# Performance work log

Measured on AMD Instinct MI355X. Metric: run time of the kernel, lower is better.

The kernel has to match this reference:

```python
import jax, jax.numpy as jnp
import numpy as np

# Dimensions (source globals scaled to production: r=256 residues, s=128 sequences)
S, R, CM, CZ, C, H = 128, 256, 256, 128, 32, 8
EPS = 1e-5  # torch LayerNorm default


def setup_inputs() -> dict:
    key = jax.random.key(0)
    ks = jax.random.split(key, 14)
    msa = jax.random.normal(ks[0], (S, R, CM), dtype=jnp.float32)
    pair = jax.random.normal(ks[1], (R, R, CZ), dtype=jnp.float32)
    u = lambda k, shape, fan: jax.random.uniform(k, shape, jnp.float32, -1.0 / np.sqrt(fan), 1.0 / np.sqrt(fan))
    return {
        "msa": msa,
        "pair": pair,
        # per-head LayerNorm affine params (stacked over head axis)
        "ln_msa_g": 1.0 + 0.1 * jax.random.normal(ks[2], (H, CM), dtype=jnp.float32),
        "ln_msa_b": 0.1 * jax.random.normal(ks[3], (H, CM), dtype=jnp.float32),
        "ln_pair_g": 1.0 + 0.1 * jax.random.normal(ks[4], (H, CZ), dtype=jnp.float32),
        "ln_pair_b": 0.1 * jax.random.normal(ks[5], (H, CZ), dtype=jnp.float32),
        # per-head projections (torch Linear without bias; stored as (in, out))
        "Wq": u(ks[6], (H, CM, C), CM),
        "Wk": u(ks[7], (H, CM, C), CM),
        "Wv": u(ks[8], (H, CM, C), CM),
        "Wg": u(ks[9], (H, CM, C), CM),
        "Wb": u(ks[10], (H, CZ, S), CZ),  # linear_b: c_z -> s
        # output projection c*H -> c_m (with bias)
        "Wo": u(ks[11], (H * C, CM), H * C),
        "bo": u(ks[12], (CM,), H * C),
    }


def _forward(msa, pair, ln_msa_g, ln_msa_b, ln_pair_g, ln_pair_b, Wq, Wk, Wv, Wg, Wb, Wo, bo):
    # LayerNorm normalization is head-independent; only affine differs per head.
    mu = msa.mean(-1, keepdims=True)
    var = msa.var(-1, keepdims=True)
    nm = (msa - mu) * jax.lax.rsqrt(var + EPS)              # (S, R, CM)
    p = nm[None] * ln_msa_g[:, None, None, :] + ln_msa_b[:, None, None, :]  # (H, S, R, CM)

    q = jnp.einsum("hsrc,hcd->hsrd", p, Wq)                  # (H, S, R, C)
    k = jnp.einsum("hsrc,hcd->hsrd", p, Wk)
    v = jnp.einsum("hsrc,hcd->hsrd", p, Wv)
    g = jax.nn.sigmoid(jnp.einsum("hsrc,hcd->hsrd", p, Wg))

    pmu = pair.mean(-1, keepdims=True)
    pvar = pair.var(-1, keepdims=True)
    npair = (pair - pmu) * jax.lax.rsqrt(pvar + EPS)         # (R, R, CZ)
    pp = npair[None] * ln_pair_g[:, None, None, :] + ln_pair_b[:, None, None, :]  # (H, R, R, CZ)
    bflat = jnp.einsum("hijc,hcs->hijs", pp, Wb)             # (H, R, R, S)
    # Faithful to torch: b = linear_b(flat_pair).view(s, r, r) -- a raw
    # row-major reinterpretation (NOT a transpose).
    b = bflat.reshape(H, S, R, R)

    inv_sqrt_c = np.float32(1.0 / np.sqrt(C))
    scores = (jnp.einsum("hsid,hsjd->hsij", q, k) + b) * inv_sqrt_c  # (H, S, R, R)
    # Source softmax is over dim=-2 (the query/row axis), faithful here.
    a = jax.nn.softmax(scores, axis=-2)
    o = g * jnp.einsum("hsij,hsjd->hsid", a, v)              # (H, S, R, C)

    # concat heads on last dim: (S, R, H*C)
    cat = jnp.transpose(o, (1, 2, 0, 3)).reshape(S, R, H * C)
    return cat @ Wo + bo                                      # (S, R, CM)


def reference(msa, pair, ln_msa_g, ln_msa_b, ln_pair_g, ln_pair_b, Wq, Wk, Wv, Wg, Wb, Wo, bo):
    return _forward(msa, pair, ln_msa_g, ln_msa_b, ln_pair_g, ln_pair_b, Wq, Wk, Wv, Wg, Wb, Wo, bo)
```

## Files before the change

kernel.cpp:

```cpp
#include <hip/hip_runtime.h>
#include <hip/hip_bf16.h>


namespace {
constexpr int S_ = 128, R_ = 256, CM_ = 256, CZ_ = 128, C_ = 32, H_ = 8;
constexpr int SR_ = S_ * R_;
constexpr int RR_ = R_ * R_;
constexpr float EPS_ = 1e-5f;
constexpr float ISC_ = 0.17677669529663687f;

constexpr size_t OFF_MU_M = 0;
constexpr size_t OFF_RS_M = OFF_MU_M + SR_;
constexpr size_t OFF_MU_P = OFF_RS_M + SR_;
constexpr size_t OFF_RS_P = OFF_MU_P + RR_;
constexpr size_t OFF_WC   = OFF_RS_P + RR_;
constexpr size_t OFF_BC   = OFF_WC + (size_t)H_ * CM_ * 128;
constexpr size_t OFF_WBP  = OFF_BC + (size_t)H_ * 128;
constexpr size_t OFF_BBP  = OFF_WBP + (size_t)H_ * CZ_ * 128;
constexpr size_t F32_END  = OFF_BBP + (size_t)H_ * 128;
constexpr size_t BF_BASE  = F32_END * 4;
constexpr size_t QKVG_ELEMS = (size_t)H_ * SR_ * C_;
constexpr size_t CAT_ELEMS  = (size_t)SR_ * CM_;
constexpr size_t WBT_ELEMS  = (size_t)H_ * 128 * 128;
constexpr size_t WOT_ELEMS  = (size_t)256 * 256;
constexpr size_t NEED_BYTES =
    BF_BASE + (4 * QKVG_ELEMS + CAT_ELEMS + WBT_ELEMS + WOT_ELEMS) * 2;
}

typedef unsigned short bf_t;
typedef short s8v __attribute__((ext_vector_type(8)));
typedef float f4v __attribute__((ext_vector_type(4)));

__device__ __forceinline__ unsigned pk2(float lo, float hi) {
  __hip_bfloat162 t = __float22bfloat162_rn(float2{lo, hi});
  return *reinterpret_cast<unsigned*>(&t);
}
__device__ __forceinline__ bf_t pk1(float v) {
  __hip_bfloat16 t = __float2bfloat16(v);
  return *reinterpret_cast<bf_t*>(&t);
}
__device__ __forceinline__ float uplo(unsigned u) { return __uint_as_float(u << 16); }
__device__ __forceinline__ float uphi(unsigned u) { return __uint_as_float(u & 0xffff0000u); }
__device__ __forceinline__ void up8(uint4 u, float* f) {
  f[0] = uplo(u.x); f[1] = uphi(u.x);
  f[2] = uplo(u.y); f[3] = uphi(u.y);
  f[4] = uplo(u.z); f[5] = uphi(u.z);
  f[6] = uplo(u.w); f[7] = uphi(u.w);
}
__device__ __forceinline__ f4v mfma16(s8v a, s8v b, f4v c) {
  return __builtin_amdgcn_mfma_f32_16x16x32_bf16(a, b, c, 0, 0, 0);
}

__global__ void msa_stats_k(const float* __restrict__ msa, float* __restrict__ mu,
                            float* __restrict__ rstd) {
  int row = blockIdx.x * 4 + (threadIdx.x >> 6);
  int lane = threadIdx.x & 63;
  float4 v = reinterpret_cast<const float4*>(msa + (size_t)row * CM_)[lane];
  float s = v.x + v.y + v.z + v.w;
  float s2 = v.x * v.x + v.y * v.y + v.z * v.z + v.w * v.w;
  for (int off = 32; off; off >>= 1) {
    s += __shfl_down(s, off);
    s2 += __shfl_down(s2, off);
  }
  if (lane == 0) {
    float m = s / CM_;
    float var = s2 / CM_ - m * m;
    mu[row] = m;
    rstd[row] = rsqrtf(var + EPS_);
  }
}

__global__ void pair_stats_k(const float* __restrict__ pair, float* __restrict__ mu,
                             float* __restrict__ rstd) {
  int row = blockIdx.x * 4 + (threadIdx.x >> 6);
  int lane = threadIdx.x & 63;
  float2 v = reinterpret_cast<const float2*>(pair + (size_t)row * CZ_)[lane];
  float s = v.x + v.y;
  float s2 = v.x * v.x + v.y * v.y;
  for (int off = 32; off; off >>= 1) {
    s += __shfl_down(s, off);
    s2 += __shfl_down(s2, off);
  }
  if (lane == 0) {
    float m = s / CZ_;
    float var = s2 / CZ_ - m * m;
    mu[row] = m;
    rstd[row] = rsqrtf(var + EPS_);
  }
}

__global__ void prep_weights_k(const float* __restrict__ lng_m, const float* __restrict__ lnb_m,
                               const float* __restrict__ lng_p, const float* __restrict__ lnb_p,
                               const float* __restrict__ Wq, const float* __restrict__ Wk,
                               const float* __restrict__ Wv, const float* __restrict__ Wg,
                               const float* __restrict__ Wb, const float* __restrict__ Wo,
                               bf_t* __restrict__ wct, float* __restrict__ bc,
                               float* __restrict__ Wbp, float* __restrict__ bbp,
                               bf_t* __restrict__ wbt, bf_t* __restrict__ wot) {
  int b = blockIdx.x;
  int t = threadIdx.x;
  if (b < H_) {
    int h = b;
    int m = t >> 5, d = t & 31;
    const float* Wsrc = (m == 0) ? Wq : (m == 1) ? Wk : (m == 2) ? Wv : Wg;
    float scale = (m == 0) ? ISC_ : 1.0f;
    float bias = 0.f;
    for (int c = 0; c < CM_; c++) {
      float w = Wsrc[((size_t)h * CM_ + c) * C_ + d];
      bias += lnb_m[h * CM_ + c] * w;
      wct[((size_t)h * 128 + t) * 256 + c] = pk1(lng_m[h * CM_ + c] * w * scale);
    }
    bc[h * 128 + t] = bias * scale;
  } else if (b < 2 * H_) {
    int h = b - H_;
    float bias = 0.f;
    for (int c = 0; c < CZ_; c++) {
      float w = Wb[((size_t)h * CZ_ + c) * S_ + t];
      bias += lnb_p[h * CZ_ + c] * w;
      Wbp[((size_t)h * CZ_ + c) * 128 + t] = lng_p[h * CZ_ + c] * w * ISC_;
    }
    bbp[h * 128 + t] = bias * ISC_;
    for (int c = 0; c < CZ_; c++)
      wbt[((size_t)h * 128 + t) * 128 + c] = pk1(Wbp[((size_t)h * CZ_ + c) * 128 + t]);
  } else {
    int n = (b - 2 * H_) * 128 + t;
    for (int k = 0; k < 256; k++) wot[(size_t)n * 256 + k] = pk1(Wo[(size_t)k * 256 + n]);
  }
}

__global__ __launch_bounds__(512, 1) void qkvg_mfma_k(
    const float* __restrict__ msa, const float* __restrict__ mu, const float* __restrict__ rstd,
    const bf_t* __restrict__ wct, const float* __restrict__ bc, bf_t* __restrict__ q,
    bf_t* __restrict__ k, bf_t* __restrict__ v, bf_t* __restrict__ g) {
  __shared__ bf_t sm_a[128 * 256];
  __shared__ bf_t sm_w[128 * 256];
  int ib = blockIdx.x;
  int tid = threadIdx.x;
  int w = tid >> 6, l = tid & 63;
  int l15 = l & 15, l4 = l >> 4;
  int iw = w >> 2, jw = w & 3;
  int sr0 = ib * 128;
  int sx7 = l15 & 7;
#pragma unroll
  for (int rep = 0; rep < 8; rep++) {
    int flat = rep * 512 + tid;
    int row = flat >> 5, c = flat & 31;
    int srow = sr0 + row;
    const float4* ps = reinterpret_cast<const float4*>(msa + (size_t)srow * CM_ + c * 8);
    float4 x0 = ps[0], x1 = ps[1];
    float m = mu[srow], rs = rstd[srow];
    uint4 wv;
    wv.x = pk2((x0.x - m) * rs, (x0.y - m) * rs);
    wv.y = pk2((x0.z - m) * rs, (x0.w - m) * rs);
    wv.z = pk2((x1.x - m) * rs, (x1.y - m) * rs);
    wv.w = pk2((x1.z - m) * rs, (x1.w - m) * rs);
    *reinterpret_cast<uint4*>(&sm_a[row * 256 + ((c ^ (row & 7)) << 3)]) = wv;
  }
  for (int h = 0; h < H_; h++) {
    __syncthreads();
#pragma unroll
    for (int rep = 0; rep < 8; rep++) {
      int flat = rep * 512 + tid;
      int row = flat >> 5, c = flat & 31;
      *reinterpret_cast<uint4*>(&sm_w[row * 256 + ((c ^ (row & 7)) << 3)]) =
          *reinterpret_cast<const uint4*>(wct + ((size_t)h * 128 + row) * 256 + c * 8);
    }
    f4v acc[4][2];
#pragma unroll
    for (int jt = 0; jt < 2; jt++) {
      float bb = bc[h * 128 + jw * 32 + jt * 16 + l15];
#pragma unroll
      for (int it = 0; it < 4; it++) acc[it][jt] = f4v{bb, bb, bb, bb};
    }
    __syncthreads();
#pragma unroll
    for (int ks = 0; ks < 8; ks++) {
      int ch = ks * 4 + l4;
      s8v a[4], b[2];
#pragma unroll
      for (int it = 0; it < 4; it++)
        a[it] = *reinterpret_cast<const s8v*>(
            &sm_a[(iw * 64 + it * 16 + l15) * 256 + ((ch ^ sx7) << 3)]);
#pragma unroll
      for (int jt = 0; jt < 2; jt++)
        b[jt] = *reinterpret_cast<const s8v*>(
            &sm_w[(jw * 32 + jt * 16 + l15) * 256 + ((ch ^ sx7) << 3)]);
#pragma unroll
      for (int it = 0; it < 4; it++)
#pragma unroll
        for (int jt = 0; jt < 2; jt++) acc[it][jt] = mfma16(a[it], b[jt], acc[it][jt]);
    }
#pragma unroll
    for (int it = 0; it < 4; it++) {
#pragma unroll
      for (int jt = 0; jt < 2; jt++) {
        int j = jw * 32 + jt * 16 + l15;
        int m_ = j >> 5, d = j & 31;
        bf_t* dst = (m_ == 0) ? q : (m_ == 1) ? k : (m_ == 2) ? v : g;
#pragma unroll
        for (int r = 0; r < 4; r++) {
          int i = iw * 64 + it * 16 + l4 * 4 + r;
          float val = acc[it][jt][r];
          if (m_ == 3) val = 1.f / (1.f + __expf(-val));
          dst[((size_t)h * SR_ + sr0 + i) * C_ + d] = pk1(val);
        }
      }
    }
  }
}

__global__ __launch_bounds__(512, 1) void attn_mfma_k(
    const float* __restrict__ pair, const float* __restrict__ mu_p,
    const float* __restrict__ rs_p, const bf_t* __restrict__ wbt,
    const float* __restrict__ bbp, const bf_t* __restrict__ qg, const bf_t* __restrict__ kg,
    const bf_t* __restrict__ vg, const bf_t* __restrict__ gg, bf_t* __restrict__ cat) {
  __shared__ bf_t sm_pN[256 * 128];
  __shared__ bf_t sm_wt[64 * 128];
  __shared__ bf_t sm_p[256 * 64];
  __shared__ bf_t sm_q[256 * 40];
  __shared__ bf_t sm_k[64 * 40];
  __shared__ bf_t sm_vt[32 * 64];
  __shared__ float sm_redm[4 * 64];
  __shared__ float sm_reds[4 * 64];

  int s = blockIdx.x, h = blockIdx.y;
  int tid = threadIdx.x;
  int w = tid >> 6, l = tid & 63;
  int l15 = l & 15, l4 = l >> 4;
  int iw = w >> 1, jw = w & 1;
  int iw2 = w >> 1, dw = w & 1;
  size_t base = ((size_t)h * SR_ + (size_t)s * R_) * C_;

#pragma unroll
  for (int rep = 0; rep < 2; rep++) {
    int flat = rep * 512 + tid;
    int row = flat >> 2, c = flat & 3;
    *reinterpret_cast<uint4*>(&sm_q[row * 40 + c * 8]) =
        *reinterpret_cast<const uint4*>(qg + base + (size_t)row * C_ + c * 8);
  }

  f4v accO[4];
#pragma unroll
  for (int it = 0; it < 4; it++) accO[it] = f4v{0.f, 0.f, 0.f, 0.f};

  for (int p = 0; p < 2; p++) {
    __syncthreads();
#pragma unroll
    for (int rep = 0; rep < 8; rep++) {
      int flat = rep * 512 + tid;
      int row = flat >> 4, c = flat & 15;
      int gr = (2 * s + (row >> 7)) * 256 + 2 * (row & 127) + p;
      const float4* ps = reinterpret_cast<const float4*>(pair + (size_t)gr * CZ_) + c * 2;
      float4 x0 = ps[0], x1 = ps[1];
      float m = mu_p[gr], rs = rs_p[gr];
      uint4 wv;
      wv.x = pk2((x0.x - m) * rs, (x0.y - m) * rs);
      wv.y = pk2((x0.z - m) * rs, (x0.w - m) * rs);
      wv.z = pk2((x1.x - m) * rs, (x1.y - m) * rs);
      wv.w = pk2((x1.z - m) * rs, (x1.w - m) * rs);
      *reinterpret_cast<uint4*>(&sm_pN[row * 128 + ((c ^ (row & 7)) << 3)]) = wv;
    }
    for (int jh = 0; jh < 2; jh++) {
      int j0 = p * 128 + jh * 64;
      __syncthreads();
#pragma unroll
      for (int rep = 0; rep < 2; rep++) {
        int flat = rep * 512 + tid;
        int row = flat >> 4, c = flat & 15;
        *reinterpret_cast<uint4*>(&sm_wt[row * 128 + ((c ^ (row & 7)) << 3)]) =
            *reinterpret_cast<const uint4*>(wbt + ((size_t)h * 128 + jh * 64 + row) * 128 +
                                            c * 8);
      }
      if (tid < 256) {
        int row = tid >> 2, c = tid & 3;
        *reinterpret_cast<uint4*>(&sm_k[row * 40 + c * 8]) =
            *reinterpret_cast<const uint4*>(kg + base + (size_t)(j0 + row) * C_ + c * 8);
      } else {
        int t2 = tid - 256;
        int j = t2 >> 2, dc = t2 & 3;
        uint4 u = *reinterpret_cast<const uint4*>(vg + base + (size_t)(j0 + j) * C_ + dc * 8);
        unsigned uu[4] = {u.x, u.y, u.z, u.w};
#pragma unroll
        for (int e = 0; e < 8; e++) {
          int d = dc * 8 + e;
          bf_t val = (bf_t)((uu[e >> 1] >> ((e & 1) * 16)) & 0xffff);
          sm_vt[d * 64 + ((((j >> 3) ^ (d & 7)) << 3) + (j & 7))] = val;
        }
      }
      f4v acc[4][2];
      {
        float bb0 = bbp[h * 128 + jh * 64 + jw * 32 + l15];
        float bb1 = bbp[h * 128 + jh * 64 + jw * 32 + 16 + l15];
#pragma unroll
        for (int it = 0; it < 4; it++) {
          acc[it][0] = f4v{bb0, bb0, bb0, bb0};
          acc[it][1] = f4v{bb1, bb1, bb1, bb1};
        }
      }
      __syncthreads();
      int sx7 = l15 & 7;
#pragma unroll
      for (int ks = 0; ks < 4; ks++) {
        int ch = (ks * 4 + l4);
        s8v a[4], b[2];
#pragma unroll
        for (int it = 0; it < 4; it++)
          a[it] = *reinterpret_cast<const s8v*>(
              &sm_pN[(iw * 64 + it * 16 + l15) * 128 + ((ch ^ sx7) << 3)]);
#pragma unroll
        for (int u = 0; u < 2; u++)
          b[u] = *reinterpret_cast<const s8v*>(
              &sm_wt[(jw * 32 + u * 16 + l15) * 128 + ((ch ^ sx7) << 3)]);
#pragma unroll
        for (int it = 0; it < 4; it++) {
          acc[it][0] = mfma16(a[it], b[0], acc[it][0]);
          acc[it][1] = mfma16(a[it], b[1], acc[it][1]);
        }
      }
      {
        s8v qa[4], kb[2];
#pragma unroll
        for (int it = 0; it < 4; it++)
          qa[it] = *reinterpret_cast<const s8v*>(&sm_q[(iw * 64 + it * 16 + l15) * 40 + l4 * 8]);
#pragma unroll
        for (int u = 0; u < 2; u++)
          kb[u] = *reinterpret_cast<const s8v*>(&sm_k[(jw * 32 + u * 16 + l15) * 40 + l4 * 8]);
#pragma unroll
        for (int it = 0; it < 4; it++) {
          acc[it][0] = mfma16(qa[it], kb[0], acc[it][0]);
          acc[it][1] = mfma16(qa[it], kb[1], acc[it][1]);
        }
      }
      float mx[2];
#pragma unroll
      for (int u = 0; u < 2; u++) {
        float m0 = -1e30f;
#pragma unroll
        for (int it = 0; it < 4; it++)
#pragma unroll
          for (int r = 0; r < 4; r++) m0 = fmaxf(m0, acc[it][u][r]);
        m0 = fmaxf(m0, __shfl_xor(m0, 16));
        m0 = fmaxf(m0, __shfl_xor(m0, 32));
        mx[u] = m0;
      }
      if (l < 16) {
        sm_redm[iw * 64 + jw * 32 + l] = mx[0];
        sm_redm[iw * 64 + jw * 32 + 16 + l] = mx[1];
      }
      __syncthreads();
      float M[2], sm[2];
#pragma unroll
      for (int u = 0; u < 2; u++) {
        int jc = jw * 32 + u * 16 + l15;
        float m0 = sm_redm[jc];
        m0 = fmaxf(m0, sm_redm[64 + jc]);
        m0 = fmaxf(m0, sm_redm[128 + jc]);
        m0 = fmaxf(m0, sm_redm[192 + jc]);
        M[u] = m0;
        float s0 = 0.f;
#pragma unroll
        for (int it = 0; it < 4; it++) {
#pragma unroll
          for (int r = 0; r < 4; r++) {
            float e = __expf(acc[it][u][r] - m0);
            acc[it][u][r] = e;
            s0 += e;
          }
        }
        s0 += __shfl_xor(s0, 16);
        s0 += __shfl_xor(s0, 32);
        sm[u] = s0;
      }
      if (l < 16) {
        sm_reds[iw * 64 + jw * 32 + l] = sm[0];
        sm_reds[iw * 64 + jw * 32 + 16 + l] = sm[1];
      }
      __syncthreads();
#pragma unroll
      for (int u = 0; u < 2; u++) {
        int jc = jw * 32 + u * 16 + l15;
        float tot = sm_reds[jc] + sm_reds[64 + jc] + sm_reds[128 + jc] + sm_reds[192 + jc];
        float inv = 1.0f / tot;
#pragma unroll
        for (int it = 0; it < 4; it++) {
#pragma unroll
          for (int r = 0; r < 4; r++) {
            int i = iw * 64 + it * 16 + l4 * 4 + r;
            sm_p[i * 64 + ((((jc >> 3) ^ (i & 7)) << 3) + (jc & 7))] = pk1(acc[it][u][r] * inv);
          }
        }
      }
      __syncthreads();
#pragma unroll
      for (int ks = 0; ks < 2; ks++) {
        int ch = ks * 4 + l4;
        s8v vb = *reinterpret_cast<const s8v*>(
            &sm_vt[(dw * 16 + l15) * 64 + ((ch ^ sx7) << 3)]);
#pragma unroll
        for (int it = 0; it < 4; it++) {
          s8v pa = *reinterpret_cast<const s8v*>(
              &sm_p[(iw2 * 64 + it * 16 + l15) * 64 + ((ch ^ sx7) << 3)]);
          accO[it] = mfma16(pa, vb, accO[it]);
        }
      }
    }
  }
#pragma unroll
  for (int it = 0; it < 4; it++) {
#pragma unroll
    for (int r = 0; r < 4; r++) {
      int i = iw2 * 64 + it * 16 + l4 * 4 + r;
      int d = dw * 16 + l15;
      float gf = uplo((unsigned)gg[base + (size_t)i * C_ + d]);
      cat[((size_t)s * R_ + i) * 256 + h * 32 + d] = pk1(accO[it][r] * gf);
    }
  }
}

__global__ __launch_bounds__(512, 1) void out_mfma_k(const bf_t* __restrict__ cat,
                                                     const bf_t* __restrict__ wot,
                                                     const float* __restrict__ bo,
                                                     float* __restrict__ out) {
  __shared__ bf_t sm_a[128 * 256];
  __shared__ bf_t sm_b[128 * 256];
  int ib = blockIdx.x;
  int tid = threadIdx.x;
  int w = tid >> 6, l = tid & 63;
  int l15 = l & 15, l4 = l >> 4, sx7 = l15 & 7;
  int iw = w >> 2, jw = w & 3;
  int sr0 = ib * 128;
#pragma unroll
  for (int rep = 0; rep < 8; rep++) {
    int flat = rep * 512 + tid;
    int row = flat >> 5, c = flat & 31;
    *reinterpret_cast<uint4*>(&sm_a[row * 256 + ((c ^ (row & 7)) << 3)]) =
        *reinterpret_cast<const uint4*>(cat + (size_t)(sr0 + row) * 256 + c * 8);
  }
  for (int nb = 0; nb < 2; nb++) {
    __syncthreads();
#pragma unroll
    for (int rep = 0; rep < 8; rep++) {
      int flat = rep * 512 + tid;
      int row = flat >> 5, c = flat & 31;
      *reinterpret_cast<uint4*>(&sm_b[row * 256 + ((c ^ (row & 7)) << 3)]) =
          *reinterpret_cast<const uint4*>(wot + (size_t)(nb * 128 + row) * 256 + c * 8);
    }
    f4v acc[4][2];
#pragma unroll
    for (int jt = 0; jt < 2; jt++) {
      float bb = bo[nb * 128 + jw * 32 + jt * 16 + l15];
#pragma unroll
      for (int it = 0; it < 4; it++) acc[it][jt] = f4v{bb, bb, bb, bb};
    }
    __syncthreads();
#pragma unroll
    for (int ks = 0; ks < 8; ks++) {
      int ch = ks * 4 + l4;
      s8v a[4], b[2];
#pragma unroll
      for (int it = 0; it < 4; it++)
        a[it] = *reinterpret_cast<const s8v*>(
            &sm_a[(iw * 64 + it * 16 + l15) * 256 + ((ch ^ sx7) << 3)]);
#pragma unroll
      for (int jt = 0; jt < 2; jt++)
        b[jt] = *reinterpret_cast<const s8v*>(
            &sm_b[(jw * 32 + jt * 16 + l15) * 256 + ((ch ^ sx7) << 3)]);
#pragma unroll
      for (int it = 0; it < 4; it++)
#pragma unroll
        for (int jt = 0; jt < 2; jt++) acc[it][jt] = mfma16(a[it], b[jt], acc[it][jt]);
    }
#pragma unroll
    for (int it = 0; it < 4; it++)
#pragma unroll
      for (int jt = 0; jt < 2; jt++) {
        int n = nb * 128 + jw * 32 + jt * 16 + l15;
#pragma unroll
        for (int r = 0; r < 4; r++) {
          int i = iw * 64 + it * 16 + l4 * 4 + r;
          out[(size_t)(sr0 + i) * 256 + n] = acc[it][jt][r];
        }
      }
  }
}

extern "C" void kernel_launch(void* const* d_in, const int* in_sizes, int n_in, void* d_out,
                              int out_size, void* d_ws, size_t ws_size, hipStream_t stream) {
  if (ws_size < NEED_BYTES) return;

  const float* msa = (const float*)d_in[0];
  const float* pair = (const float*)d_in[1];
  const float* lng_m = (const float*)d_in[2];
  const float* lnb_m = (const float*)d_in[3];
  const float* lng_p = (const float*)d_in[4];
  const float* lnb_p = (const float*)d_in[5];
  const float* Wq = (const float*)d_in[6];
  const float* Wk = (const float*)d_in[7];
  const float* Wv = (const float*)d_in[8];
  const float* Wg = (const float*)d_in[9];
  const float* Wb = (const float*)d_in[10];
  const float* Wo = (const float*)d_in[11];
  const float* bo = (const float*)d_in[12];
  float* out = (float*)d_out;
  float* ws = (float*)d_ws;

  float* mu_m = ws + OFF_MU_M;
  float* rs_m = ws + OFF_RS_M;
  float* mu_p = ws + OFF_MU_P;
  float* rs_p = ws + OFF_RS_P;
  bf_t* wct = (bf_t*)(ws + OFF_WC);
  float* bc = ws + OFF_BC;
  float* Wbp = ws + OFF_WBP;
  float* bbp = ws + OFF_BBP;
  bf_t* qb = (bf_t*)((char*)d_ws + BF_BASE);
  bf_t* kb = qb + QKVG_ELEMS;
  bf_t* vb = kb + QKVG_ELEMS;
  bf_t* gb = vb + QKVG_ELEMS;
  bf_t* cat = gb + QKVG_ELEMS;
  bf_t* wbt = cat + CAT_ELEMS;
  bf_t* wot = wbt + WBT_ELEMS;

  msa_stats_k<<<SR_ / 4, 256, 0, stream>>>(msa, mu_m, rs_m);
  pair_stats_k<<<RR_ / 4, 256, 0, stream>>>(pair, mu_p, rs_p);
  prep_weights_k<<<18, 128, 0, stream>>>(lng_m, lnb_m, lng_p, lnb_p, Wq, Wk, Wv, Wg, Wb, Wo, wct,
                                         bc, Wbp, bbp, wbt, wot);
  qkvg_mfma_k<<<SR_ / 128, 512, 0, stream>>>(msa, mu_m, rs_m, wct, bc, qb, kb, vb, gb);
  attn_mfma_k<<<dim3(S_, H_), 512, 0, stream>>>(pair, mu_p, rs_p, wbt, bbp, qb, kb, vb, gb, cat);
  out_mfma_k<<<SR_ / 128, 512, 0, stream>>>(cat, wot, bo, out);
}
```

Baseline: 182.5 us.

## Pre-normalize pair to bf16 once and parallelize weight preparation

Pair stats now produce a normalized bf16 copy of the pair tensor, so the attention kernel loads bf16 directly instead of re-reading fp32 pair plus mean/rstd and normalizing per block. Each attention block reads pair rows for every head, so this halves the bytes loaded and drops the per-element normalization work there. Weight preparation is split into a small bias kernel and a wide per-element conversion kernel, replacing 18 blocks of serial loops with 1792 blocks. The cost is an extra 16 MB bf16 workspace buffer plus its write and read.

```diff
diff --git a/kernel.cpp b/kernel.cpp
--- a/kernel.cpp
+++ b/kernel.cpp
@@ -11,9 +11,7 @@
 
 constexpr size_t OFF_MU_M = 0;
 constexpr size_t OFF_RS_M = OFF_MU_M + SR_;
-constexpr size_t OFF_MU_P = OFF_RS_M + SR_;
-constexpr size_t OFF_RS_P = OFF_MU_P + RR_;
-constexpr size_t OFF_WC   = OFF_RS_P + RR_;
+constexpr size_t OFF_WC   = OFF_RS_M + SR_;
 constexpr size_t OFF_BC   = OFF_WC + (size_t)H_ * CM_ * 128;
 constexpr size_t OFF_WBP  = OFF_BC + (size_t)H_ * 128;
 constexpr size_t OFF_BBP  = OFF_WBP + (size_t)H_ * CZ_ * 128;
@@ -23,8 +21,9 @@
 constexpr size_t CAT_ELEMS  = (size_t)SR_ * CM_;
 constexpr size_t WBT_ELEMS  = (size_t)H_ * 128 * 128;
 constexpr size_t WOT_ELEMS  = (size_t)256 * 256;
+constexpr size_t PAIRN_ELEMS = (size_t)RR_ * 128;
 constexpr size_t NEED_BYTES =
-    BF_BASE + (4 * QKVG_ELEMS + CAT_ELEMS + WBT_ELEMS + WOT_ELEMS) * 2;
+    BF_BASE + (4 * QKVG_ELEMS + CAT_ELEMS + WBT_ELEMS + WOT_ELEMS + PAIRN_ELEMS) * 2;
 }
 
 typedef unsigned short bf_t;
@@ -41,15 +40,10 @@
 }
 __device__ __forceinline__ float uplo(unsigned u) { return __uint_as_float(u << 16); }
 __device__ __forceinline__ float uphi(unsigned u) { return __uint_as_float(u & 0xffff0000u); }
-__device__ __forceinline__ void up8(uint4 u, float* f) {
-  f[0] = uplo(u.x); f[1] = uphi(u.x);
-  f[2] = uplo(u.y); f[3] = uphi(u.y);
-  f[4] = uplo(u.z); f[5] = uphi(u.z);
-  f[6] = uplo(u.w); f[7] = uphi(u.w);
-}
 __device__ __forceinline__ f4v mfma16(s8v a, s8v b, f4v c) {
   return __builtin_amdgcn_mfma_f32_16x16x32_bf16(a, b, c, 0, 0, 0);
 }
+__device__ __forceinline__ s8v ld8(const bf_t* p) { return *reinterpret_cast<const s8v*>(p); }
 
 __global__ void msa_stats_k(const float* __restrict__ msa, float* __restrict__ mu,
                             float* __restrict__ rstd) {
@@ -70,33 +64,29 @@
   }
 }
 
-__global__ void pair_stats_k(const float* __restrict__ pair, float* __restrict__ mu,
-                             float* __restrict__ rstd) {
-  int row = blockIdx.x * 4 + (threadIdx.x >> 6);
+__global__ __launch_bounds__(512) void pair_norm_k(const float* __restrict__ pair,
+                                                   bf_t* __restrict__ pairN) {
+  int row = blockIdx.x * 8 + (threadIdx.x >> 6);
   int lane = threadIdx.x & 63;
   float2 v = reinterpret_cast<const float2*>(pair + (size_t)row * CZ_)[lane];
   float s = v.x + v.y;
   float s2 = v.x * v.x + v.y * v.y;
   for (int off = 32; off; off >>= 1) {
-    s += __shfl_down(s, off);
-    s2 += __shfl_down(s2, off);
-  }
-  if (lane == 0) {
-    float m = s / CZ_;
-    float var = s2 / CZ_ - m * m;
-    mu[row] = m;
-    rstd[row] = rsqrtf(var + EPS_);
-  }
-}
-
-__global__ void prep_weights_k(const float* __restrict__ lng_m, const float* __restrict__ lnb_m,
-                               const float* __restrict__ lng_p, const float* __restrict__ lnb_p,
-                               const float* __restrict__ Wq, const float* __restrict__ Wk,
-                               const float* __restrict__ Wv, const float* __restrict__ Wg,
-                               const float* __restrict__ Wb, const float* __restrict__ Wo,
-                               bf_t* __restrict__ wct, float* __restrict__ bc,
-                               float* __restrict__ Wbp, float* __restrict__ bbp,
-                               bf_t* __restrict__ wbt, bf_t* __restrict__ wot) {
+    s += __shfl_xor(s, off);
+    s2 += __shfl_xor(s2, off);
+  }
+  float m = s / CZ_;
+  float var = s2 / CZ_ - m * m;
+  float rs = rsqrtf(var + EPS_);
+  reinterpret_cast<unsigned*>(pairN)[(size_t)row * 64 + lane] =
+      pk2((v.x - m) * rs, (v.y - m) * rs);
+}
+
+__global__ void prep_small_k(const float* __restrict__ lnb_m, const float* __restrict__ lnb_p,
+                             const float* __restrict__ Wq, const float* __restrict__ Wk,
+                             const float* __restrict__ Wv, const float* __restrict__ Wg,
+                             const float* __restrict__ Wb, float* __restrict__ bc,
+                             float* __restrict__ bbp) {
   int b = blockIdx.x;
   int t = threadIdx.x;
   if (b < H_) {
@@ -105,26 +95,38 @@
     const float* Wsrc = (m == 0) ? Wq : (m == 1) ? Wk : (m == 2) ? Wv : Wg;
     float scale = (m == 0) ? ISC_ : 1.0f;
     float bias = 0.f;
-    for (int c = 0; c < CM_; c++) {
-      float w = Wsrc[((size_t)h * CM_ + c) * C_ + d];
-      bias += lnb_m[h * CM_ + c] * w;
-      wct[((size_t)h * 128 + t) * 256 + c] = pk1(lng_m[h * CM_ + c] * w * scale);
-    }
+    for (int c = 0; c < CM_; c++) bias += lnb_m[h * CM_ + c] * Wsrc[((size_t)h * CM_ + c) * C_ + d];
     bc[h * 128 + t] = bias * scale;
-  } else if (b < 2 * H_) {
+  } else {
     int h = b - H_;
     float bias = 0.f;
-    for (int c = 0; c < CZ_; c++) {
-      float w = Wb[((size_t)h * CZ_ + c) * S_ + t];
-      bias += lnb_p[h * CZ_ + c] * w;
-      Wbp[((size_t)h * CZ_ + c) * 128 + t] = lng_p[h * CZ_ + c] * w * ISC_;
-    }
+    for (int c = 0; c < CZ_; c++) bias += lnb_p[h * CZ_ + c] * Wb[((size_t)h * CZ_ + c) * S_ + t];
     bbp[h * 128 + t] = bias * ISC_;
-    for (int c = 0; c < CZ_; c++)
-      wbt[((size_t)h * 128 + t) * 128 + c] = pk1(Wbp[((size_t)h * CZ_ + c) * 128 + t]);
+  }
+}
+
+__global__ __launch_bounds__(256) void prep_wide_k(
+    const float* __restrict__ lng_m, const float* __restrict__ lng_p,
+    const float* __restrict__ Wq, const float* __restrict__ Wk, const float* __restrict__ Wv,
+    const float* __restrict__ Wg, const float* __restrict__ Wb, const float* __restrict__ Wo,
+    bf_t* __restrict__ wct, bf_t* __restrict__ wbt, bf_t* __restrict__ wot) {
+  int idx = blockIdx.x * 256 + threadIdx.x;
+  if (idx < 262144) {
+    int h = idx >> 15, rem = idx & 32767;
+    int j = rem >> 8, c = rem & 255;
+    int m = j >> 5, d = j & 31;
+    const float* Wsrc = (m == 0) ? Wq : (m == 1) ? Wk : (m == 2) ? Wv : Wg;
+    float scale = (m == 0) ? ISC_ : 1.0f;
+    wct[idx] = pk1(lng_m[h * CM_ + c] * Wsrc[((size_t)h * CM_ + c) * C_ + d] * scale);
+  } else if (idx < 262144 + 131072) {
+    int i2 = idx - 262144;
+    int h = i2 >> 14, rem = i2 & 16383;
+    int t = rem >> 7, c = rem & 127;
+    wbt[i2] = pk1(lng_p[h * CZ_ + c] * Wb[((size_t)h * CZ_ + c) * S_ + t] * ISC_);
   } else {
-    int n = (b - 2 * H_) * 128 + t;
-    for (int k = 0; k < 256; k++) wot[(size_t)n * 256 + k] = pk1(Wo[(size_t)k * 256 + n]);
+    int i3 = idx - 262144 - 131072;
+    int n = i3 >> 8, k = i3 & 255;
+    wot[i3] = pk1(Wo[(size_t)k * 256 + n]);
   }
 }
 
@@ -179,12 +181,10 @@
       s8v a[4], b[2];
 #pragma unroll
       for (int it = 0; it < 4; it++)
-        a[it] = *reinterpret_cast<const s8v*>(
-            &sm_a[(iw * 64 + it * 16 + l15) * 256 + ((ch ^ sx7) << 3)]);
+        a[it] = ld8(&sm_a[(iw * 64 + it * 16 + l15) * 256 + ((ch ^ sx7) << 3)]);
 #pragma unroll
       for (int jt = 0; jt < 2; jt++)
-        b[jt] = *reinterpret_cast<const s8v*>(
-            &sm_w[(jw * 32 + jt * 16 + l15) * 256 + ((ch ^ sx7) << 3)]);
+        b[jt] = ld8(&sm_w[(jw * 32 + jt * 16 + l15) * 256 + ((ch ^ sx7) << 3)]);
 #pragma unroll
       for (int it = 0; it < 4; it++)
 #pragma unroll
@@ -210,8 +210,7 @@
 }
 
 __global__ __launch_bounds__(512, 1) void attn_mfma_k(
-    const float* __restrict__ pair, const float* __restrict__ mu_p,
-    const float* __restrict__ rs_p, const bf_t* __restrict__ wbt,
+    const bf_t* __restrict__ pairN, const bf_t* __restrict__ wbt,
     const float* __restrict__ bbp, const bf_t* __restrict__ qg, const bf_t* __restrict__ kg,
     const bf_t* __restrict__ vg, const bf_t* __restrict__ gg, bf_t* __restrict__ cat) {
   __shared__ bf_t sm_pN[256 * 128];
@@ -250,15 +249,8 @@
       int flat = rep * 512 + tid;
       int row = flat >> 4, c = flat & 15;
       int gr = (2 * s + (row >> 7)) * 256 + 2 * (row & 127) + p;
-      const float4* ps = reinterpret_cast<const float4*>(pair + (size_t)gr * CZ_) + c * 2;
-      float4 x0 = ps[0], x1 = ps[1];
-      float m = mu_p[gr], rs = rs_p[gr];
-      uint4 wv;
-      wv.x = pk2((x0.x - m) * rs, (x0.y - m) * rs);
-      wv.y = pk2((x0.z - m) * rs, (x0.w - m) * rs);
-      wv.z = pk2((x1.x - m) * rs, (x1.y - m) * rs);
-      wv.w = pk2((x1.z - m) * rs, (x1.w - m) * rs);
-      *reinterpret_cast<uint4*>(&sm_pN[row * 128 + ((c ^ (row & 7)) << 3)]) = wv;
+      *reinterpret_cast<uint4*>(&sm_pN[row * 128 + ((c ^ (row & 7)) << 3)]) =
+          *reinterpret_cast<const uint4*>(pairN + (size_t)gr * 128 + c * 8);
     }
     for (int jh = 0; jh < 2; jh++) {
       int j0 = p * 128 + jh * 64;
@@ -305,12 +297,10 @@
         s8v a[4], b[2];
 #pragma unroll
         for (int it = 0; it < 4; it++)
-          a[it] = *reinterpret_cast<const s8v*>(
-              &sm_pN[(iw * 64 + it * 16 + l15) * 128 + ((ch ^ sx7) << 3)]);
+          a[it] = ld8(&sm_pN[(iw * 64 + it * 16 + l15) * 128 + ((ch ^ sx7) << 3)]);
 #pragma unroll
         for (int u = 0; u < 2; u++)
-          b[u] = *reinterpret_cast<const s8v*>(
-              &sm_wt[(jw * 32 + u * 16 + l15) * 128 + ((ch ^ sx7) << 3)]);
+          b[u] = ld8(&sm_wt[(jw * 32 + u * 16 + l15) * 128 + ((ch ^ sx7) << 3)]);
 #pragma unroll
         for (int it = 0; it < 4; it++) {
           acc[it][0] = mfma16(a[it], b[0], acc[it][0]);
@@ -321,10 +311,10 @@
         s8v qa[4], kb[2];
 #pragma unroll
         for (int it = 0; it < 4; it++)
-          qa[it] = *reinterpret_cast<const s8v*>(&sm_q[(iw * 64 + it * 16 + l15) * 40 + l4 * 8]);
+          qa[it] = ld8(&sm_q[(iw * 64 + it * 16 + l15) * 40 + l4 * 8]);
 #pragma unroll
         for (int u = 0; u < 2; u++)
-          kb[u] = *reinterpret_cast<const s8v*>(&sm_k[(jw * 32 + u * 16 + l15) * 40 + l4 * 8]);
+          kb[u] = ld8(&sm_k[(jw * 32 + u * 16 + l15) * 40 + l4 * 8]);
 #pragma unroll
         for (int it = 0; it < 4; it++) {
           acc[it][0] = mfma16(qa[it], kb[0], acc[it][0]);
@@ -394,12 +384,10 @@
 #pragma unroll
       for (int ks = 0; ks < 2; ks++) {
         int ch = ks * 4 + l4;
-        s8v vb = *reinterpret_cast<const s8v*>(
-            &sm_vt[(dw * 16 + l15) * 64 + ((ch ^ sx7) << 3)]);
+        s8v vb = ld8(&sm_vt[(dw * 16 + l15) * 64 + ((ch ^ sx7) << 3)]);
 #pragma unroll
         for (int it = 0; it < 4; it++) {
-          s8v pa = *reinterpret_cast<const s8v*>(
-              &sm_p[(iw2 * 64 + it * 16 + l15) * 64 + ((ch ^ sx7) << 3)]);
+          s8v pa = ld8(&sm_p[(iw2 * 64 + it * 16 + l15) * 64 + ((ch ^ sx7) << 3)]);
           accO[it] = mfma16(pa, vb, accO[it]);
         }
       }
@@ -459,12 +447,10 @@
       s8v a[4], b[2];
 #pragma unroll
       for (int it = 0; it < 4; it++)
-        a[it] = *reinterpret_cast<const s8v*>(
-            &sm_a[(iw * 64 + it * 16 + l15) * 256 + ((ch ^ sx7) << 3)]);
+        a[it] = ld8(&sm_a[(iw * 64 + it * 16 + l15) * 256 + ((ch ^ sx7) << 3)]);
 #pragma unroll
       for (int jt = 0; jt < 2; jt++)
-        b[jt] = *reinterpret_cast<const s8v*>(
-            &sm_b[(jw * 32 + jt * 16 + l15) * 256 + ((ch ^ sx7) << 3)]);
+        b[jt] = ld8(&sm_b[(jw * 32 + jt * 16 + l15) * 256 + ((ch ^ sx7) << 3)]);
 #pragma unroll
       for (int it = 0; it < 4; it++)
 #pragma unroll
@@ -506,11 +492,8 @@
 
   float* mu_m = ws + OFF_MU_M;
   float* rs_m = ws + OFF_RS_M;
-  float* mu_p = ws + OFF_MU_P;
-  float* rs_p = ws + OFF_RS_P;
   bf_t* wct = (bf_t*)(ws + OFF_WC);
   float* bc = ws + OFF_BC;
-  float* Wbp = ws + OFF_WBP;
   float* bbp = ws + OFF_BBP;
   bf_t* qb = (bf_t*)((char*)d_ws + BF_BASE);
   bf_t* kb = qb + QKVG_ELEMS;
@@ -519,12 +502,13 @@
   bf_t* cat = gb + QKVG_ELEMS;
   bf_t* wbt = cat + CAT_ELEMS;
   bf_t* wot = wbt + WBT_ELEMS;
+  bf_t* pairN = wot + WOT_ELEMS;
 
   msa_stats_k<<<SR_ / 4, 256, 0, stream>>>(msa, mu_m, rs_m);
-  pair_stats_k<<<RR_ / 4, 256, 0, stream>>>(pair, mu_p, rs_p);
-  prep_weights_k<<<18, 128, 0, stream>>>(lng_m, lnb_m, lng_p, lnb_p, Wq, Wk, Wv, Wg, Wb, Wo, wct,
-                                         bc, Wbp, bbp, wbt, wot);
+  pair_norm_k<<<RR_ / 8, 512, 0, stream>>>(pair, pairN);
+  prep_small_k<<<2 * H_, 128, 0, stream>>>(lnb_m, lnb_p, Wq, Wk, Wv, Wg, Wb, bc, bbp);
+  prep_wide_k<<<1792, 256, 0, stream>>>(lng_m, lng_p, Wq, Wk, Wv, Wg, Wb, Wo, wct, wbt, wot);
   qkvg_mfma_k<<<SR_ / 128, 512, 0, stream>>>(msa, mu_m, rs_m, wct, bc, qb, kb, vb, gb);
-  attn_mfma_k<<<dim3(S_, H_), 512, 0, stream>>>(pair, mu_p, rs_p, wbt, bbp, qb, kb, vb, gb, cat);
+  attn_mfma_k<<<dim3(S_, H_), 512, 0, stream>>>(pairN, wbt, bbp, qb, kb, vb, gb, cat);
   out_mfma_k<<<SR_ / 128, 512, 0, stream>>>(cat, wot, bo, out);
 }
```

Measured after the change: 173.7 us. 1.05x faster.
